# Kernel optimization log

Hardware: AMD Instinct MI355X
Metric: run time of the kernel (lower is better)

Reference implementation:

```python
import jax, jax.numpy as jnp
import numpy as np
from jax import lax

B, L = 4, 1024
D_MODEL = 512
D_INNER = 2 * D_MODEL            # expand=2 -> 1024
HEADDIM = 64
NHEADS = D_INNER // HEADDIM      # 16
D_STATE = 64
D_CONV = 4
NLAYERS = 2
NTOKEN = 60695
PAD_IDX = 60694
NCLS = 164
CONV_DIM = D_INNER + 2 * D_STATE            # 1152 (ngroups=1)
D_IN_PROJ = 2 * D_INNER + 2 * D_STATE + NHEADS  # 2192
MAX_VALUE = 512.0
EPS = 1e-5


def _ln(x, g=None, b=None):
    m = jnp.mean(x, -1, keepdims=True)
    v = jnp.mean((x - m) ** 2, -1, keepdims=True)
    y = (x - m) * lax.rsqrt(v + EPS)
    return y if g is None else y * g + b


def _smart_flip(X, pad_mask):
    # reverse only the valid (non-pad) prefix of each sequence
    lengths = (~pad_mask).sum(1)
    rng = jnp.arange(X.shape[1])[None, :]
    flip = rng < lengths[:, None]
    pos = jnp.where(flip, lengths[:, None] - 1 - rng, rng)
    return jnp.take_along_axis(X, pos[:, :, None], axis=1)


def _mamba2(u, in_w, conv_w, conv_b, A_log, dt_bias, Dskip, norm_w, out_w):
    # Mamba2 block (mamba_ssm defaults: ngroups=1, silu conv act, gated RMSNorm)
    Bb, Ll, _ = u.shape
    zxbcdt = u @ in_w.T                                      # (B,L,D_IN_PROJ)
    z = zxbcdt[..., :D_INNER]
    xBC = zxbcdt[..., D_INNER:D_INNER + CONV_DIM]
    dt = jax.nn.softplus(zxbcdt[..., -NHEADS:] + dt_bias)    # (B,L,H)
    # causal depthwise conv1d + silu
    xBC = jnp.pad(xBC, ((0, 0), (D_CONV - 1, 0), (0, 0))).transpose(0, 2, 1)
    xBC = lax.conv_general_dilated(xBC, conv_w[:, None, :], (1,), 'VALID',
                                   feature_group_count=CONV_DIM)
    xBC = jax.nn.silu(xBC.transpose(0, 2, 1) + conv_b)       # (B,L,CONV_DIM)
    x = xBC[..., :D_INNER].reshape(Bb, Ll, NHEADS, HEADDIM)
    Bm = xBC[..., D_INNER:D_INNER + D_STATE]                 # (B,L,N)
    Cm = xBC[..., D_INNER + D_STATE:]                        # (B,L,N)
    dA = jnp.exp(dt * (-jnp.exp(A_log)))                     # (B,L,H)

    def step(h, t):
        dA_t, dt_t, x_t, B_t, C_t = t
        # h: (B,H,P,N)
        h = h * dA_t[:, :, None, None] \
            + (dt_t[:, :, None] * x_t)[..., None] * B_t[:, None, None, :]
        y = jnp.einsum('bhpn,bn->bhp', h, C_t)
        return h, y

    h0 = jnp.zeros((Bb, NHEADS, HEADDIM, D_STATE), u.dtype)
    xs = (dA.transpose(1, 0, 2), dt.transpose(1, 0, 2),
          x.transpose(1, 0, 2, 3), Bm.transpose(1, 0, 2), Cm.transpose(1, 0, 2))
    _, ys = lax.scan(step, h0, xs)                            # (L,B,H,P)
    y = ys.transpose(1, 0, 2, 3) + Dskip[None, None, :, None] * x
    y = y.reshape(Bb, Ll, D_INNER)
    y = y * jax.nn.silu(z)                                    # gated RMSNorm
    y = y * lax.rsqrt(jnp.mean(y * y, -1, keepdims=True) + EPS) * norm_w
    return y @ out_w.T


def _forward(src, values, pad_mask, embed, ge_ln_g, ge_ln_b,
             ve_w1, ve_b1, ve_w2, ve_b2, ve_ln_g, ve_ln_b,
             in_proj_w, conv_w_f, conv_b_f, A_log_f, dt_bias_f, D_f, norm_w_f,
             conv_w_r, conv_b_r, A_log_r, dt_bias_r, D_r, norm_w_r, out_proj_w,
             expr_w1, expr_b1, expr_w2, expr_b2, expr_w3, expr_b3,
             cls_w1, cls_b1, cls_ln1_g, cls_ln1_b, cls_w2, cls_b2,
             cls_ln2_g, cls_ln2_b, cls_wo, cls_bo):
    src_emb = _ln(embed[src], ge_ln_g, ge_ln_b)
    v = jnp.minimum(values, MAX_VALUE)[..., None]
    v = jax.nn.relu(v @ ve_w1.T + ve_b1)
    v = _ln(v @ ve_w2.T + ve_b2, ve_ln_g, ve_ln_b)
    h = (src_emb + v) * (~pad_mask)[..., None]
    for i in range(NLAYERS):
        hn = _ln(h)  # F.layer_norm without affine
        out = _mamba2(hn, in_proj_w[i], conv_w_f[i], conv_b_f[i], A_log_f[i],
                      dt_bias_f[i], D_f[i], norm_w_f[i], out_proj_w[i])
        rev = _smart_flip(hn, pad_mask)
        out_r = _mamba2(rev, in_proj_w[i], conv_w_r[i], conv_b_r[i], A_log_r[i],
                        dt_bias_r[i], D_r[i], norm_w_r[i], out_proj_w[i])
        out_r = _smart_flip(out_r, pad_mask)
        h = _ln((out + out_r) / 2)
    # ExprDecoder (MLM head)
    e = jax.nn.leaky_relu(h @ expr_w1.T + expr_b1)
    e = jax.nn.leaky_relu(e @ expr_w2.T + expr_b2)
    mlm = (e @ expr_w3.T + expr_b3)[..., 0]
    # cell embedding: cls token
    cell = h[:, 0, :]
    # ClsDecoder
    c = _ln(jax.nn.relu(cell @ cls_w1.T + cls_b1), cls_ln1_g, cls_ln1_b)
    c = _ln(jax.nn.relu(c @ cls_w2.T + cls_b2), cls_ln2_g, cls_ln2_b)
    cls = c @ cls_wo.T + cls_bo
    return mlm, cell, cls


def setup_inputs() -> dict:
    key = jax.random.key(0)
    ks = iter(jax.random.split(key, 64))
    w = lambda *s: jax.random.normal(next(ks), s, jnp.float32) * 0.02
    embed = w(NTOKEN, D_MODEL).at[PAD_IDX].set(0.0)
    dt_u = jax.random.uniform(next(ks), (NLAYERS, NHEADS), minval=1e-3, maxval=0.1)
    dt_u2 = jax.random.uniform(next(ks), (NLAYERS, NHEADS), minval=1e-3, maxval=0.1)
    return dict(
        src=jax.random.randint(next(ks), (B, L), 0, PAD_IDX),
        values=jax.random.uniform(next(ks), (B, L), jnp.float32),
        src_key_padding_mask=jnp.zeros((B, L), bool),
        embed=embed,
        ge_ln_g=jnp.ones((D_MODEL,)), ge_ln_b=jnp.zeros((D_MODEL,)),
        ve_w1=w(D_MODEL, 1), ve_b1=jnp.zeros((D_MODEL,)),
        ve_w2=w(D_MODEL, D_MODEL), ve_b2=jnp.zeros((D_MODEL,)),
        ve_ln_g=jnp.ones((D_MODEL,)), ve_ln_b=jnp.zeros((D_MODEL,)),
        in_proj_w=w(NLAYERS, D_IN_PROJ, D_MODEL),
        conv_w_f=w(NLAYERS, CONV_DIM, D_CONV), conv_b_f=jnp.zeros((NLAYERS, CONV_DIM)),
        A_log_f=jnp.log(jax.random.uniform(next(ks), (NLAYERS, NHEADS), minval=1.0, maxval=16.0)),
        dt_bias_f=dt_u + jnp.log(-jnp.expm1(-dt_u)),
        D_f=jnp.ones((NLAYERS, NHEADS)), norm_w_f=jnp.ones((NLAYERS, D_INNER)),
        conv_w_r=w(NLAYERS, CONV_DIM, D_CONV), conv_b_r=jnp.zeros((NLAYERS, CONV_DIM)),
        A_log_r=jnp.log(jax.random.uniform(next(ks), (NLAYERS, NHEADS), minval=1.0, maxval=16.0)),
        dt_bias_r=dt_u2 + jnp.log(-jnp.expm1(-dt_u2)),
        D_r=jnp.ones((NLAYERS, NHEADS)), norm_w_r=jnp.ones((NLAYERS, D_INNER)),
        out_proj_w=w(NLAYERS, D_MODEL, D_INNER),
        expr_w1=w(D_MODEL, D_MODEL), expr_b1=jnp.zeros((D_MODEL,)),
        expr_w2=w(D_MODEL, D_MODEL), expr_b2=jnp.zeros((D_MODEL,)),
        expr_w3=w(1, D_MODEL), expr_b3=jnp.zeros((1,)),
        cls_w1=w(D_MODEL, D_MODEL), cls_b1=jnp.zeros((D_MODEL,)),
        cls_ln1_g=jnp.ones((D_MODEL,)), cls_ln1_b=jnp.zeros((D_MODEL,)),
        cls_w2=w(D_MODEL, D_MODEL), cls_b2=jnp.zeros((D_MODEL,)),
        cls_ln2_g=jnp.ones((D_MODEL,)), cls_ln2_b=jnp.zeros((D_MODEL,)),
        cls_wo=w(NCLS, D_MODEL), cls_bo=jnp.zeros((NCLS,)),
    )


def reference(src, values, src_key_padding_mask, embed, ge_ln_g, ge_ln_b,
              ve_w1, ve_b1, ve_w2, ve_b2, ve_ln_g, ve_ln_b,
              in_proj_w, conv_w_f, conv_b_f, A_log_f, dt_bias_f, D_f, norm_w_f,
              conv_w_r, conv_b_r, A_log_r, dt_bias_r, D_r, norm_w_r, out_proj_w,
              expr_w1, expr_b1, expr_w2, expr_b2, expr_w3, expr_b3,
              cls_w1, cls_b1, cls_ln1_g, cls_ln1_b, cls_w2, cls_b2,
              cls_ln2_g, cls_ln2_b, cls_wo, cls_bo):
    return _forward(src, values, src_key_padding_mask, embed, ge_ln_g, ge_ln_b,
                    ve_w1, ve_b1, ve_w2, ve_b2, ve_ln_g, ve_ln_b,
                    in_proj_w, conv_w_f, conv_b_f, A_log_f, dt_bias_f, D_f, norm_w_f,
                    conv_w_r, conv_b_r, A_log_r, dt_bias_r, D_r, norm_w_r, out_proj_w,
                    expr_w1, expr_b1, expr_w2, expr_b2, expr_w3, expr_b3,
                    cls_w1, cls_b1, cls_ln1_g, cls_ln1_b, cls_w2, cls_b2,
                    cls_ln2_g, cls_ln2_b, cls_wo, cls_bo)
```

## Files before the change

kernel.cpp:

```cpp
#include <hip/hip_runtime.h>
#include <hip/hip_bf16.h>
#include <math.h>

constexpr int Bb = 4, Ls = 1024, DM = 512, DI = 1024, NH = 16, HD = 64, DS = 64;
constexpr int CDIM = DI + 2 * DS;
constexpr int DIP  = 2 * DI + 2 * DS + NH;
constexpr int NPJ  = 2 * DI + 2 * DS;
constexpr float EPSf = 1e-5f;
constexpr int TOK = Bb * Ls;
constexpr int CH = 64, NCH = Ls / CH;

#define DEVI __device__ __forceinline__

using bfrag = __attribute__((ext_vector_type(8))) short;
using f4v   = __attribute__((ext_vector_type(4))) float;
using u16x8 = __attribute__((ext_vector_type(8))) unsigned short;

#define GLOAD16(gp, lp)                                                              \
  __builtin_amdgcn_global_load_lds((__attribute__((address_space(1))) void*)(gp),   \
                                   (__attribute__((address_space(3))) void*)(lp),   \
                                   16, 0, 0)

DEVI float wsum(float v) {
#pragma unroll
  for (int o = 32; o > 0; o >>= 1) v += __shfl_xor(v, o);
  return v;
}
DEVI float sigmoidf_(float x) { return 1.f / (1.f + __expf(-x)); }
DEVI unsigned short f2bf(float x) {
  union { float f; unsigned u; } c{x};
  unsigned u = c.u;
  u += 0x7fffu + ((u >> 16) & 1u);
  return (unsigned short)(u >> 16);
}
DEVI float bf2f(unsigned short u) {
  union { unsigned u; float f; } c{(unsigned)u << 16};
  return c.f;
}

DEVI void ld8(const float* __restrict__ p, int lane, float (&x)[8]) {
  float4 a = *(const float4*)(p + lane * 4);
  float4 b = *(const float4*)(p + 256 + lane * 4);
  x[0] = a.x; x[1] = a.y; x[2] = a.z; x[3] = a.w;
  x[4] = b.x; x[5] = b.y; x[6] = b.z; x[7] = b.w;
}
DEVI void ld8bf(const unsigned short* __restrict__ p, int lane, float (&x)[8]) {
  ushort4 a = *(const ushort4*)(p + lane * 4);
  ushort4 b = *(const ushort4*)(p + 256 + lane * 4);
  x[0] = bf2f(a.x); x[1] = bf2f(a.y); x[2] = bf2f(a.z); x[3] = bf2f(a.w);
  x[4] = bf2f(b.x); x[5] = bf2f(b.y); x[6] = bf2f(b.z); x[7] = bf2f(b.w);
}
DEVI void st8(float* __restrict__ p, int lane, const float (&x)[8]) {
  *(float4*)(p + lane * 4) = make_float4(x[0], x[1], x[2], x[3]);
  *(float4*)(p + 256 + lane * 4) = make_float4(x[4], x[5], x[6], x[7]);
}
DEVI void st8bf(unsigned short* __restrict__ p, int lane, const float (&x)[8]) {
  *(ushort4*)(p + lane * 4) = make_ushort4(f2bf(x[0]), f2bf(x[1]), f2bf(x[2]), f2bf(x[3]));
  *(ushort4*)(p + 256 + lane * 4) = make_ushort4(f2bf(x[4]), f2bf(x[5]), f2bf(x[6]), f2bf(x[7]));
}
DEVI void norm8(float (&x)[8]) {
  float s = 0;
#pragma unroll
  for (int j = 0; j < 8; ++j) s += x[j];
  float mean = wsum(s) * (1.f / 512.f);
#pragma unroll
  for (int j = 0; j < 8; ++j) x[j] -= mean;
  float q = 0;
#pragma unroll
  for (int j = 0; j < 8; ++j) q += x[j] * x[j];
  float var = wsum(q) * (1.f / 512.f);
  float inv = rsqrtf(var + EPSf);
#pragma unroll
  for (int j = 0; j < 8; ++j) x[j] *= inv;
}

__global__ __launch_bounds__(256) void k_w2bf(const float* __restrict__ in,
                                              unsigned short* __restrict__ out, int n8) {
  int i = blockIdx.x * 256 + threadIdx.x;
  if (i >= n8) return;
  const float4* p = (const float4*)in + (size_t)i * 2;
  float4 a = p[0], b = p[1];
  *((ushort4*)out + (size_t)i * 2) = make_ushort4(f2bf(a.x), f2bf(a.y), f2bf(a.z), f2bf(a.w));
  *((ushort4*)out + (size_t)i * 2 + 1) = make_ushort4(f2bf(b.x), f2bf(b.y), f2bf(b.z), f2bf(b.w));
}

__global__ __launch_bounds__(256) void k_embed(const int* __restrict__ src, const float* __restrict__ values,
    const float* __restrict__ embed, const float* __restrict__ gg, const float* __restrict__ gb,
    const float* __restrict__ vw1, const float* __restrict__ vb1,
    float* __restrict__ hbuf, unsigned short* __restrict__ v1bf) {
  int gw = (blockIdx.x * 256 + threadIdx.x) >> 6;
  int lane = threadIdx.x & 63;
  if (gw >= TOK) return;
  const float* er = embed + (size_t)src[gw] * DM;
  float x[8];
  ld8(er, lane, x);
  norm8(x);
  float g[8], bv[8];
  ld8(gg, lane, g); ld8(gb, lane, bv);
#pragma unroll
  for (int j = 0; j < 8; ++j) x[j] = x[j] * g[j] + bv[j];
  st8(hbuf + (size_t)gw * DM, lane, x);
  float val = fminf(values[gw], 512.f);
  float w1[8], b1[8];
  ld8(vw1, lane, w1); ld8(vb1, lane, b1);
  float v[8];
#pragma unroll
  for (int j = 0; j < 8; ++j) v[j] = fmaxf(val * w1[j] + b1[j], 0.f);
  st8bf(v1bf + (size_t)gw * DM, lane, v);
}

__global__ __launch_bounds__(256) void k_haddv(const float* __restrict__ t2, const float* __restrict__ g,
    const float* __restrict__ bb, const unsigned char* __restrict__ mask, float* __restrict__ hbuf) {
  int gw = (blockIdx.x * 256 + threadIdx.x) >> 6;
  int lane = threadIdx.x & 63;
  if (gw >= TOK) return;
  float x[8];
  ld8(t2 + (size_t)gw * DM, lane, x);
  norm8(x);
  float gv[8], bv[8], h[8];
  ld8(g, lane, gv); ld8(bb, lane, bv);
  ld8(hbuf + (size_t)gw * DM, lane, h);
  float mf = mask[gw] ? 0.f : 1.f;
#pragma unroll
  for (int j = 0; j < 8; ++j) h[j] = (h[j] + x[j] * gv[j] + bv[j]) * mf;
  st8(hbuf + (size_t)gw * DM, lane, h);
}

__global__ __launch_bounds__(256) void k_lndt(const float* __restrict__ h, const float* __restrict__ inw,
    const float* __restrict__ dtbF, const float* __restrict__ AlogF,
    const float* __restrict__ dtbR, const float* __restrict__ AlogR,
    const int* __restrict__ len, unsigned short* __restrict__ hnbf,
    float* __restrict__ dtf, float* __restrict__ laf,
    float* __restrict__ dtr, float* __restrict__ lar) {
  int gw = (blockIdx.x * 256 + threadIdx.x) >> 6;
  int lane = threadIdx.x & 63;
  if (gw >= TOK) return;
  float x[8];
  ld8(h + (size_t)gw * DM, lane, x);
  norm8(x);
  st8bf(hnbf + (size_t)gw * DM, lane, x);
  const float* wdt = inw + (size_t)NPJ * DM;
  float myraw = 0.f;
#pragma unroll
  for (int hh = 0; hh < NH; ++hh) {
    float w[8];
    ld8(wdt + (size_t)hh * DM, lane, w);
    float s = 0;
#pragma unroll
    for (int j = 0; j < 8; ++j) s += x[j] * w[j];
    s = wsum(s);
    if (lane == hh) myraw = s;
  }
  if (lane < NH) {
    int t = gw & (Ls - 1), b = gw >> 10;
    int ln = len[b];
    int pos = (t < ln) ? (ln - 1 - t) : t;
    size_t grev = (size_t)(b * Ls + pos);
    float rf = myraw + dtbF[lane];
    float df = rf > 20.f ? rf : log1pf(__expf(rf));
    dtf[(size_t)gw * NH + lane] = df;
    laf[(size_t)gw * NH + lane] = -__expf(AlogF[lane]) * df;
    float rr = myraw + dtbR[lane];
    float dr = rr > 20.f ? rr : log1pf(__expf(rr));
    dtr[grev * NH + lane] = dr;
    lar[grev * NH + lane] = -__expf(AlogR[lane]) * dr;
  }
}

template <int ACT, int OMODE>
__global__ __launch_bounds__(256) void gemm_bf(const unsigned short* __restrict__ A,
    const unsigned short* __restrict__ W, const float* __restrict__ bias,
    void* __restrict__ Cout, int M, int N, int K) {
  constexpr int BK = 64;
  __shared__ unsigned short As[128 * BK];
  __shared__ unsigned short Bs[128 * BK];
  int tid = threadIdx.x;
  int bm = blockIdx.y * 128, bn = blockIdx.x * 128;
  int wv = tid >> 6, lane = tid & 63;
  int mb = (wv >> 1) * 64, nb = (wv & 1) * 64;
  int rA = lane >> 3;
  int cswz = (lane & 7) ^ rA;
  f4v acc[4][4] = {};

  for (int k0 = 0; k0 < K; k0 += BK) {
#pragma unroll
    for (int q = 0; q < 4; ++q) {
      int ch = wv * 4 + q;
      const unsigned short* ga = A + (size_t)(bm + ch * 8 + rA) * K + k0 + cswz * 8;
      GLOAD16(ga, &As[ch * 512]);
      const unsigned short* gb = W + (size_t)(bn + ch * 8 + rA) * K + k0 + cswz * 8;
      GLOAD16(gb, &Bs[ch * 512]);
    }
    __syncthreads();
#pragma unroll
    for (int ks = 0; ks < BK; ks += 32) {
      int kb = (ks >> 3) + (lane >> 4);
      bfrag af[4], bg[4];
#pragma unroll
      for (int i = 0; i < 4; ++i) {
        int ra_ = mb + i * 16 + (lane & 15);
        af[i] = *(const bfrag*)((const char*)As + ((ra_ * 128 + kb * 16) ^ ((ra_ & 7) << 4)));
        int rb_ = nb + i * 16 + (lane & 15);
        bg[i] = *(const bfrag*)((const char*)Bs + ((rb_ * 128 + kb * 16) ^ ((rb_ & 7) << 4)));
      }
#pragma unroll
      for (int i = 0; i < 4; ++i)
#pragma unroll
        for (int j = 0; j < 4; ++j)
          acc[i][j] = __builtin_amdgcn_mfma_f32_16x16x32_bf16(af[i], bg[j], acc[i][j], 0, 0, 0);
    }
    __syncthreads();
  }

  int cb = bn + nb + (lane & 15);
  int rb = bm + mb + ((lane >> 4) << 2);
#pragma unroll
  for (int j = 0; j < 4; ++j) {
    float bv = bias ? bias[cb + j * 16] : 0.f;
#pragma unroll
    for (int i = 0; i < 4; ++i) {
#pragma unroll
      for (int r = 0; r < 4; ++r) {
        float v = acc[i][j][r] + bv;
        if (ACT == 1) v = fmaxf(v, 0.f);
        if (ACT == 2) v = v > 0.f ? v : 0.01f * v;
        size_t idx = (size_t)(rb + i * 16 + r) * N + cb + j * 16;
        if (OMODE == 0) ((float*)Cout)[idx] = v;
        else ((unsigned short*)Cout)[idx] = f2bf(v);
      }
    }
  }
}

__global__ __launch_bounds__(256) void k_convbc(const unsigned short* __restrict__ zx,
    const float* __restrict__ cwF, const float* __restrict__ cbF,
    const float* __restrict__ cwR, const float* __restrict__ cbR,
    const int* __restrict__ len, unsigned short* __restrict__ bcbuf) {
  int idx = blockIdx.x * 256 + threadIdx.x;
  if (idx >= 2 * TOK * 128) return;
  int col = idx & 127;
  int bt = (idx >> 7) & (TOK - 1);
  int dir = idx >> 19;
  int b = bt >> 10, t = bt & (Ls - 1);
  int ln = len[b];
  const float* cw = dir ? cwR : cwF;
  const float* cb = dir ? cbR : cbF;
  int ccd = DI + col;
  float4 w4 = *(const float4*)(cw + ccd * 4);
  float s = cb[ccd];
  float wk[4] = {w4.x, w4.y, w4.z, w4.w};
#pragma unroll
  for (int k = 0; k < 4; ++k) {
    int rl = t - 3 + k;
    if (rl >= 0) {
      int gr = dir ? (rl < ln ? ln - 1 - rl : rl) : rl;
      s += wk[k] * bf2f(zx[((size_t)(b * Ls + gr)) * NPJ + 2 * DI + col]);
    }
  }
  s = s * sigmoidf_(s);
  bcbuf[idx] = f2bf(s);
}

__global__ __launch_bounds__(256) void k_chunk(const unsigned short* __restrict__ zx,
    const unsigned short* __restrict__ bcbuf,
    const float* __restrict__ cwF, const float* __restrict__ cbF,
    const float* __restrict__ cwR, const float* __restrict__ cbR,
    const float* __restrict__ dtF, const float* __restrict__ laF,
    const float* __restrict__ dtR, const float* __restrict__ laR,
    const float* __restrict__ DkF, const float* __restrict__ DkR,
    const int* __restrict__ len,
    float* __restrict__ yF, float* __restrict__ yR,
    float* __restrict__ gbuf, float* __restrict__ cumbuf) {
  __shared__ unsigned short Cb[4096], Bbs[4096], BbT[4096], xT[4096], Wt[4096];
  __shared__ float ldsL[64], sdt_[64], fs[64];
  int blk2 = blockIdx.x;
  int dir = blk2 >> 10;
  int blk = blk2 & 1023;
  int c = blk & 15, bh = blk >> 4, h = bh & 15, b = bh >> 4;
  int tid = threadIdx.x, wv = tid >> 6, lane = tid & 63;
  int c0 = c * CH;
  int ln = len[b];
  const float* cw = dir ? cwR : cwF;
  const float* cbias = dir ? cbR : cbF;
  const float* dtp = dir ? dtR : dtF;
  const float* ldap = dir ? laR : laF;
  float Dh = (dir ? DkR : DkF)[h];
  float* y = dir ? yR : yF;

  if (tid < 64) {
    size_t off = ((size_t)(b * Ls + c0 + tid)) * NH + h;
    float dtv = dtp[off];
    float v = ldap[off];
#pragma unroll
    for (int o = 1; o < 64; o <<= 1) {
      float n = __shfl_up(v, o);
      if (tid >= o) v += n;
    }
    ldsL[tid] = v;
    sdt_[tid] = dtv;
    cumbuf[(size_t)blk2 * 64 + tid] = __expf(v);
    float L63 = __shfl(v, 63);
    fs[tid] = __expf(L63 - v) * dtv;
  }
  __syncthreads();

  {
    const unsigned short* bc = bcbuf + ((size_t)(dir * TOK + b * Ls + c0)) * 128;
    int r = tid >> 2;
    int colq = (tid & 3) * 32;
#pragma unroll
    for (int g = 0; g < 2; ++g) {
      int col = colq + g * 16;
      u16x8 v0 = *(const u16x8*)(bc + (size_t)r * 128 + col);
      u16x8 v1 = *(const u16x8*)(bc + (size_t)r * 128 + col + 8);
      if (col < 64) {
        *(u16x8*)((char*)Bbs + ((r * 128 + col * 2) ^ ((r & 7) << 4))) = v0;
        *(u16x8*)((char*)Bbs + ((r * 128 + col * 2 + 16) ^ ((r & 7) << 4))) = v1;
      } else {
        int n = col - 64;
        *(u16x8*)((char*)Cb + ((r * 128 + n * 2) ^ ((r & 7) << 4))) = v0;
        *(u16x8*)((char*)Cb + ((r * 128 + n * 2 + 16) ^ ((r & 7) << 4))) = v1;
      }
    }
  }
  {
    int n = tid & 63;
    int tg = (tid >> 6) * 16;
    const unsigned short* bc = bcbuf + ((size_t)(dir * TOK + b * Ls + c0 + tg)) * 128 + n;
    float vals[16];
#pragma unroll
    for (int t = 0; t < 16; ++t) vals[t] = bf2f(bc[(size_t)t * 128]) * fs[tg + t];
#pragma unroll
    for (int hv = 0; hv < 2; ++hv) {
      u16x8 pk;
#pragma unroll
      for (int k = 0; k < 8; ++k) pk[k] = f2bf(vals[hv * 8 + k]);
      *(u16x8*)((char*)BbT + ((n * 128 + (tg + hv * 8) * 2) ^ ((n & 7) << 4))) = pk;
    }
  }
  {
    int cch = tid & 63;
    int tg = (tid >> 6) * 16;
    int gcol = DI + h * 64 + cch;
    int ccd = h * 64 + cch;
    float4 w4 = *(const float4*)(cw + ccd * 4);
    float bias = cbias[ccd];
    float vv[19];
#pragma unroll
    for (int k = 0; k < 19; ++k) {
      int rl = c0 + tg - 3 + k;
      float val = 0.f;
      if (rl >= 0) {
        int gr = dir ? (rl < ln ? ln - 1 - rl : rl) : rl;
        val = bf2f(zx[((size_t)(b * Ls + gr)) * NPJ + gcol]);
      }
      vv[k] = val;
    }
    int p = cch;
#pragma unroll
    for (int hv = 0; hv < 2; ++hv) {
      u16x8 pk;
#pragma unroll
      for (int k = 0; k < 8; ++k) {
        int t = hv * 8 + k;
        float s = bias + w4.x * vv[t] + w4.y * vv[t + 1] + w4.z * vv[t + 2] + w4.w * vv[t + 3];
        pk[k] = f2bf(s * sigmoidf_(s));
      }
      *(u16x8*)((char*)xT + ((p * 128 + (tg + hv * 8) * 2) ^ ((p & 7) << 4))) = pk;
    }
  }
  __syncthreads();

  f4v accS[4] = {};
#pragma unroll
  for (int ks = 0; ks < 64; ks += 32) {
    int kb = (ks >> 3) + (lane >> 4);
    int ra = wv * 16 + (lane & 15);
    bfrag af = *(const bfrag*)((const char*)Cb + ((ra * 128 + kb * 16) ^ ((ra & 7) << 4)));
#pragma unroll
    for (int j = 0; j < 4; ++j) {
      int rb = j * 16 + (lane & 15);
      bfrag bg = *(const bfrag*)((const char*)Bbs + ((rb * 128 + kb * 16) ^ ((rb & 7) << 4)));
      accS[j] = __builtin_amdgcn_mfma_f32_16x16x32_bf16(af, bg, accS[j], 0, 0, 0);
    }
  }
  {
    int trow = wv * 16 + ((lane >> 4) << 2);
#pragma unroll
    for (int j = 0; j < 4; ++j) {
      int s = j * 16 + (lane & 15);
      float ds = sdt_[s], Lsv = ldsL[s];
#pragma unroll
      for (int r = 0; r < 4; ++r) {
        int tt = trow + r;
        float wval = (s <= tt) ? accS[j][r] * ds * __expf(ldsL[tt] - Lsv) : 0.f;
        *(unsigned short*)((char*)Wt + ((tt * 128 + s * 2) ^ ((tt & 7) << 4))) = f2bf(wval);
      }
    }
  }
  __syncthreads();

  f4v accY[4] = {}, accG[4] = {};
#pragma unroll
  for (int ks = 0; ks < 64; ks += 32) {
    int kb = (ks >> 3) + (lane >> 4);
    int ra = wv * 16 + (lane & 15);
    bfrag afW = *(const bfrag*)((const char*)Wt + ((ra * 128 + kb * 16) ^ ((ra & 7) << 4)));
    bfrag afB = *(const bfrag*)((const char*)BbT + ((ra * 128 + kb * 16) ^ ((ra & 7) << 4)));
#pragma unroll
    for (int j = 0; j < 4; ++j) {
      int rb = j * 16 + (lane & 15);
      bfrag bg = *(const bfrag*)((const char*)xT + ((rb * 128 + kb * 16) ^ ((rb & 7) << 4)));
      accY[j] = __builtin_amdgcn_mfma_f32_16x16x32_bf16(afW, bg, accY[j], 0, 0, 0);
      accG[j] = __builtin_amdgcn_mfma_f32_16x16x32_bf16(afB, bg, accG[j], 0, 0, 0);
    }
  }
  int trow = wv * 16 + ((lane >> 4) << 2);
#pragma unroll
  for (int j = 0; j < 4; ++j) {
    int p = j * 16 + (lane & 15);
#pragma unroll
    for (int r = 0; r < 4; ++r) {
      int t = trow + r;
      float xval = bf2f(*(const unsigned short*)((const char*)xT + ((p * 128 + t * 2) ^ ((p & 7) << 4))));
      y[((size_t)(b * Ls + c0 + t)) * DI + h * 64 + p] = accY[j][r] + Dh * xval;
      gbuf[((size_t)blk2 * 64 + t) * 64 + p] = accG[j][r];
    }
  }
}

__global__ __launch_bounds__(256) void k_chain(float* __restrict__ gbuf, const float* __restrict__ cumbuf) {
  int bh = blockIdx.x;
  int tid = threadIdx.x;
  size_t base = (size_t)bh * NCH * 4096;
  float4 hv[4] = {};
  float4 g[4], gn[4];
#pragma unroll
  for (int k = 0; k < 4; ++k) g[k] = *(const float4*)(gbuf + base + (size_t)k * 1024 + tid * 4);
  float Pc = cumbuf[(size_t)bh * NCH * 64 + 63];
  for (int c = 0; c < NCH; ++c) {
    float Pn = 0.f;
    if (c + 1 < NCH) {
      Pn = cumbuf[((size_t)bh * NCH + c + 1) * 64 + 63];
#pragma unroll
      for (int k = 0; k < 4; ++k)
        gn[k] = *(const float4*)(gbuf + base + (size_t)(c + 1) * 4096 + (size_t)k * 1024 + tid * 4);
    }
#pragma unroll
    for (int k = 0; k < 4; ++k) {
      *(float4*)(gbuf + base + (size_t)c * 4096 + (size_t)k * 1024 + tid * 4) = hv[k];
      hv[k].x = fmaf(Pc, hv[k].x, g[k].x);
      hv[k].y = fmaf(Pc, hv[k].y, g[k].y);
      hv[k].z = fmaf(Pc, hv[k].z, g[k].z);
      hv[k].w = fmaf(Pc, hv[k].w, g[k].w);
      g[k] = gn[k];
    }
    Pc = Pn;
  }
}

__global__ __launch_bounds__(256) void k_corr(const unsigned short* __restrict__ bcbuf,
    const float* __restrict__ hin, const float* __restrict__ cumbuf,
    float* __restrict__ yF, float* __restrict__ yR) {
  int blk2 = blockIdx.x;
  int c = blk2 & 15;
  if (c == 0) return;
  __shared__ unsigned short Ct[4096], HT[4096];
  __shared__ float cdl[64];
  int dir = blk2 >> 10;
  int bh = (blk2 & 1023) >> 4, h = bh & 15, b = bh >> 4;
  int tid = threadIdx.x, wv = tid >> 6, lane = tid & 63;
  int c0 = c * CH;
  float* y = dir ? yR : yF;
  {
    int r = tid >> 2;
    int colq = (tid & 3) * 16;
    const unsigned short* bc = bcbuf + ((size_t)(dir * TOK + b * Ls + c0 + r)) * 128 + 64 + colq;
    u16x8 v0 = *(const u16x8*)bc;
    u16x8 v1 = *(const u16x8*)(bc + 8);
    *(u16x8*)((char*)Ct + ((r * 128 + colq * 2) ^ ((r & 7) << 4))) = v0;
    *(u16x8*)((char*)Ct + ((r * 128 + colq * 2 + 16) ^ ((r & 7) << 4))) = v1;
  }
  {
    int n = tid >> 2, p0 = (tid & 3) * 16;
    const float* hr = hin + (size_t)blk2 * 4096 + (size_t)n * 64 + p0;
#pragma unroll
    for (int q = 0; q < 4; ++q) {
      float4 v = *(const float4*)(hr + q * 4);
      float va[4] = {v.x, v.y, v.z, v.w};
#pragma unroll
      for (int k = 0; k < 4; ++k) {
        int p = p0 + q * 4 + k;
        *(unsigned short*)((char*)HT + ((p * 128 + n * 2) ^ ((p & 7) << 4))) = f2bf(va[k]);
      }
    }
  }
  if (tid < 64) cdl[tid] = cumbuf[(size_t)blk2 * 64 + tid];
  __syncthreads();

  f4v acc[4] = {};
#pragma unroll
  for (int ks = 0; ks < 64; ks += 32) {
    int kb = (ks >> 3) + (lane >> 4);
    int ra = wv * 16 + (lane & 15);
    bfrag af = *(const bfrag*)((const char*)Ct + ((ra * 128 + kb * 16) ^ ((ra & 7) << 4)));
#pragma unroll
    for (int j = 0; j < 4; ++j) {
      int rb = j * 16 + (lane & 15);
      bfrag bg = *(const bfrag*)((const char*)HT + ((rb * 128 + kb * 16) ^ ((rb & 7) << 4)));
      acc[j] = __builtin_amdgcn_mfma_f32_16x16x32_bf16(af, bg, acc[j], 0, 0, 0);
    }
  }
  int trow = wv * 16 + ((lane >> 4) << 2);
#pragma unroll
  for (int j = 0; j < 4; ++j) {
    int p = j * 16 + (lane & 15);
#pragma unroll
    for (int r = 0; r < 4; ++r) {
      int t = trow + r;
      float* yp = &y[((size_t)(b * Ls + c0 + t)) * DI + h * 64 + p];
      *yp += cdl[t] * acc[j][r];
    }
  }
}

__global__ __launch_bounds__(256) void k_gab(const float* __restrict__ yF, const float* __restrict__ yR,
    const unsigned short* __restrict__ zxb, const float* __restrict__ nwF, const float* __restrict__ nwR,
    const int* __restrict__ len, unsigned short* __restrict__ ybf) {
  int w = (blockIdx.x * 256 + threadIdx.x) >> 6;
  int lane = threadIdx.x & 63;
  if (w >= TOK) return;
  int t = w & (Ls - 1), b = w >> 10;
  int ln = len[b];
  int r = b * Ls + ((t < ln) ? (ln - 1 - t) : t);
  const float* yf = yF + (size_t)w * DI;
  const float* yr = yR + (size_t)r * DI;
  const unsigned short* zr = zxb + (size_t)w * NPJ;
  float gf[16], gr[16];
  float ssf = 0.f, ssr = 0.f;
#pragma unroll
  for (int q = 0; q < 4; ++q) {
    float4 yv = *(const float4*)(yf + lane * 4 + q * 256);
    float4 rv = *(const float4*)(yr + lane * 4 + q * 256);
    ushort4 zu = *(const ushort4*)(zr + lane * 4 + q * 256);
    float z0 = bf2f(zu.x), z1 = bf2f(zu.y), z2 = bf2f(zu.z), z3 = bf2f(zu.w);
    float s0 = z0 * sigmoidf_(z0), s1 = z1 * sigmoidf_(z1), s2 = z2 * sigmoidf_(z2), s3 = z3 * sigmoidf_(z3);
    gf[4 * q + 0] = yv.x * s0; gf[4 * q + 1] = yv.y * s1; gf[4 * q + 2] = yv.z * s2; gf[4 * q + 3] = yv.w * s3;
    gr[4 * q + 0] = rv.x * s0; gr[4 * q + 1] = rv.y * s1; gr[4 * q + 2] = rv.z * s2; gr[4 * q + 3] = rv.w * s3;
#pragma unroll
    for (int j = 0; j < 4; ++j) {
      ssf += gf[4 * q + j] * gf[4 * q + j];
      ssr += gr[4 * q + j] * gr[4 * q + j];
    }
  }
  ssf = wsum(ssf);
  ssr = wsum(ssr);
  float scf = 0.5f * rsqrtf(ssf * (1.f / (float)DI) + EPSf);
  float scr = 0.5f * rsqrtf(ssr * (1.f / (float)DI) + EPSf);
#pragma unroll
  for (int q = 0; q < 4; ++q) {
    float4 nf = *(const float4*)(nwF + lane * 4 + q * 256);
    float4 nr = *(const float4*)(nwR + lane * 4 + q * 256);
    float o0 = gf[4 * q + 0] * scf * nf.x + gr[4 * q + 0] * scr * nr.x;
    float o1 = gf[4 * q + 1] * scf * nf.y + gr[4 * q + 1] * scr * nr.y;
    float o2 = gf[4 * q + 2] * scf * nf.z + gr[4 * q + 2] * scr * nr.z;
    float o3 = gf[4 * q + 3] * scf * nf.w + gr[4 * q + 3] * scr * nr.w;
    *(ushort4*)(ybf + (size_t)w * DI + lane * 4 + q * 256) =
        make_ushort4(f2bf(o0), f2bf(o1), f2bf(o2), f2bf(o3));
  }
}

__global__ __launch_bounds__(256) void k_hln(const float* __restrict__ src, float* __restrict__ dst,
                                             unsigned short* __restrict__ dstbf) {
  int gw = (blockIdx.x * 256 + threadIdx.x) >> 6;
  int lane = threadIdx.x & 63;
  if (gw >= TOK) return;
  float x[8];
  ld8(src + (size_t)gw * DM, lane, x);
  norm8(x);
  st8(dst + (size_t)gw * DM, lane, x);
  st8bf(dstbf + (size_t)gw * DM, lane, x);
}

__global__ __launch_bounds__(256) void k_lengths(const unsigned char* __restrict__ mask, int* __restrict__ len) {
  int b = blockIdx.x;
  int tid = threadIdx.x;
  int cnt = 0;
  for (int t = tid; t < Ls; t += 256) cnt += mask[b * Ls + t] ? 0 : 1;
#pragma unroll
  for (int o = 32; o > 0; o >>= 1) cnt += __shfl_xor(cnt, o);
  __shared__ int red[4];
  if ((tid & 63) == 0) red[tid >> 6] = cnt;
  __syncthreads();
  if (tid == 0) len[b] = red[0] + red[1] + red[2] + red[3];
}

__global__ __launch_bounds__(256) void k_mlm(const unsigned short* __restrict__ e2,
                                             const float* __restrict__ w3,
                                             const float* __restrict__ b3, float* __restrict__ out) {
  int gw = (blockIdx.x * 256 + threadIdx.x) >> 6;
  int lane = threadIdx.x & 63;
  if (gw >= TOK) return;
  float x[8], w[8];
  ld8bf(e2 + (size_t)gw * DM, lane, x);
  ld8(w3, lane, w);
  float s = 0;
#pragma unroll
  for (int j = 0; j < 8; ++j) s += x[j] * w[j];
  s = wsum(s);
  if (lane == 0) out[gw] = s + b3[0];
}

__global__ __launch_bounds__(256) void k_cell(const float* __restrict__ h, float* __restrict__ out) {
  int i = blockIdx.x * 256 + threadIdx.x;
  if (i >= Bb * DM) return;
  int b = i >> 9, c = i & 511;
  out[i] = h[(size_t)b * Ls * DM + c];
}

__global__ __launch_bounds__(256) void k_clsmv(const float* __restrict__ xin, size_t xstride,
    const float* __restrict__ g, const float* __restrict__ bb, int doLN,
    const float* __restrict__ W, const float* __restrict__ bias, int doRelu,
    float* __restrict__ out, int nout) {
  int b = blockIdx.y;
  int j = blockIdx.x * 4 + (threadIdx.x >> 6);
  int lane = threadIdx.x & 63;
  if (j >= nout) return;
  float x[8];
  ld8(xin + (size_t)b * xstride, lane, x);
  if (doLN) {
    norm8(x);
    float gv[8], bv[8];
    ld8(g, lane, gv); ld8(bb, lane, bv);
#pragma unroll
    for (int k = 0; k < 8; ++k) x[k] = x[k] * gv[k] + bv[k];
  }
  float w[8];
  ld8(W + (size_t)j * DM, lane, w);
  float s = 0;
#pragma unroll
  for (int k = 0; k < 8; ++k) s += x[k] * w[k];
  s = wsum(s);
  if (lane == 0) {
    float v = s + bias[j];
    if (doRelu) v = fmaxf(v, 0.f);
    out[(size_t)b * nout + j] = v;
  }
}

constexpr size_t F_H   = 0;
constexpr size_t F_DTF = F_H + (size_t)TOK * DM;
constexpr size_t F_LAF = F_DTF + (size_t)TOK * NH;
constexpr size_t F_DTR = F_LAF + (size_t)TOK * NH;
constexpr size_t F_LAR = F_DTR + (size_t)TOK * NH;
constexpr size_t F_YF  = F_LAR + (size_t)TOK * NH;
constexpr size_t F_YR  = F_YF + (size_t)TOK * DI;
constexpr size_t F_ON  = F_YR + (size_t)TOK * DI;
constexpr size_t F_G   = F_ON + (size_t)TOK * DM;
constexpr size_t F_CUM = F_G + (size_t)2 * Bb * NH * NCH * HD * DS;
constexpr size_t F_CC1 = F_CUM + (size_t)2 * Bb * NH * NCH * 64;
constexpr size_t F_CC2 = F_CC1 + Bb * DM;
constexpr size_t F_LEN = F_CC2 + Bb * DM;
constexpr size_t F_END = F_LEN + 16;
constexpr size_t U0     = F_END * 2;
constexpr size_t UW_IN  = U0;
constexpr size_t UW_OUT = UW_IN + (size_t)2 * DIP * DM;
constexpr size_t UW_VE  = UW_OUT + (size_t)2 * DM * DI;
constexpr size_t UW_E1  = UW_VE + (size_t)DM * DM;
constexpr size_t UW_E2  = UW_E1 + (size_t)DM * DM;
constexpr size_t U_BFA  = UW_E2 + (size_t)DM * DM;
constexpr size_t U_HNBF = U_BFA + (size_t)TOK * DM;
constexpr size_t U_YBF  = U_HNBF + (size_t)TOK * DM;
constexpr size_t U_ZX   = U_YBF + (size_t)TOK * DI;
constexpr size_t U_BC   = U_ZX + (size_t)TOK * NPJ;

extern "C" void kernel_launch(void* const* d_in, const int* in_sizes, int n_in,
                              void* d_out, int out_size, void* d_ws, size_t ws_size,
                              hipStream_t stream) {
  const int* src = (const int*)d_in[0];
  const float* values = (const float*)d_in[1];
  const unsigned char* mask = (const unsigned char*)d_in[2];
  const float* embed = (const float*)d_in[3];
  const float* ge_g = (const float*)d_in[4];
  const float* ge_b = (const float*)d_in[5];
  const float* ve_w1 = (const float*)d_in[6];
  const float* ve_b1 = (const float*)d_in[7];
  const float* ve_w2 = (const float*)d_in[8];
  const float* ve_b2 = (const float*)d_in[9];
  const float* ve_g = (const float*)d_in[10];
  const float* ve_bb = (const float*)d_in[11];
  const float* in_w = (const float*)d_in[12];
  const float* conv_w_f = (const float*)d_in[13];
  const float* conv_b_f = (const float*)d_in[14];
  const float* A_f = (const float*)d_in[15];
  const float* dtb_f = (const float*)d_in[16];
  const float* D_f = (const float*)d_in[17];
  const float* nw_f = (const float*)d_in[18];
  const float* conv_w_r = (const float*)d_in[19];
  const float* conv_b_r = (const float*)d_in[20];
  const float* A_r = (const float*)d_in[21];
  const float* dtb_r = (const float*)d_in[22];
  const float* D_r = (const float*)d_in[23];
  const float* nw_r = (const float*)d_in[24];
  const float* out_w = (const float*)d_in[25];
  const float* expr_w1 = (const float*)d_in[26];
  const float* expr_b1 = (const float*)d_in[27];
  const float* expr_w2 = (const float*)d_in[28];
  const float* expr_b2 = (const float*)d_in[29];
  const float* expr_w3 = (const float*)d_in[30];
  const float* expr_b3 = (const float*)d_in[31];
  const float* cls_w1 = (const float*)d_in[32];
  const float* cls_b1 = (const float*)d_in[33];
  const float* cls_g1 = (const float*)d_in[34];
  const float* cls_bb1 = (const float*)d_in[35];
  const float* cls_w2 = (const float*)d_in[36];
  const float* cls_b2 = (const float*)d_in[37];
  const float* cls_g2 = (const float*)d_in[38];
  const float* cls_bb2 = (const float*)d_in[39];
  const float* cls_wo = (const float*)d_in[40];
  const float* cls_bo = (const float*)d_in[41];

  float* ws = (float*)d_ws;
  unsigned short* wsu = (unsigned short*)d_ws;
  float* h = ws + F_H;
  float* dtf = ws + F_DTF;
  float* laf = ws + F_LAF;
  float* dtr = ws + F_DTR;
  float* lar = ws + F_LAR;
  float* yF = ws + F_YF;
  float* yR = ws + F_YR;
  float* onew = ws + F_ON;
  float* gbuf = ws + F_G;
  float* cumb = ws + F_CUM;
  float* cc1 = ws + F_CC1;
  float* cc2 = ws + F_CC2;
  int* len = (int*)(ws + F_LEN);
  unsigned short* w_in = wsu + UW_IN;
  unsigned short* w_out = wsu + UW_OUT;
  unsigned short* w_ve = wsu + UW_VE;
  unsigned short* w_e1 = wsu + UW_E1;
  unsigned short* w_e2 = wsu + UW_E2;
  unsigned short* bfa = wsu + U_BFA;
  unsigned short* hnbf = wsu + U_HNBF;
  unsigned short* ybf = wsu + U_YBF;
  unsigned short* zxb = wsu + U_ZX;
  unsigned short* bcbuf = wsu + U_BC;
  float* t2 = onew;
  unsigned short* e2b = zxb;
  float* out = (float*)d_out;

  {
    int n;
    n = 2 * DIP * DM / 8;  k_w2bf<<<(n + 255) / 256, 256, 0, stream>>>(in_w, w_in, n);
    n = 2 * DM * DI / 8;   k_w2bf<<<(n + 255) / 256, 256, 0, stream>>>(out_w, w_out, n);
    n = DM * DM / 8;       k_w2bf<<<(n + 255) / 256, 256, 0, stream>>>(ve_w2, w_ve, n);
    n = DM * DM / 8;       k_w2bf<<<(n + 255) / 256, 256, 0, stream>>>(expr_w1, w_e1, n);
    n = DM * DM / 8;       k_w2bf<<<(n + 255) / 256, 256, 0, stream>>>(expr_w2, w_e2, n);
  }

  k_embed<<<TOK / 4, 256, 0, stream>>>(src, values, embed, ge_g, ge_b, ve_w1, ve_b1, h, bfa);
  gemm_bf<0, 0><<<dim3(DM / 128, TOK / 128), 256, 0, stream>>>(bfa, w_ve, ve_b2, t2, TOK, DM, DM);
  k_haddv<<<TOK / 4, 256, 0, stream>>>(t2, ve_g, ve_bb, mask, h);
  k_lengths<<<Bb, 256, 0, stream>>>(mask, len);

  for (int i = 0; i < 2; ++i) {
    const float* inw = in_w + (size_t)i * DIP * DM;
    unsigned short* inwb = w_in + (size_t)i * DIP * DM;
    unsigned short* outwb = w_out + (size_t)i * DM * DI;
    const float* cwF = conv_w_f + (size_t)i * CDIM * 4;
    const float* cbF = conv_b_f + (size_t)i * CDIM;
    const float* cwR = conv_w_r + (size_t)i * CDIM * 4;
    const float* cbR = conv_b_r + (size_t)i * CDIM;
    k_lndt<<<TOK / 4, 256, 0, stream>>>(h, inw, dtb_f + i * NH, A_f + i * NH,
                                        dtb_r + i * NH, A_r + i * NH, len, hnbf,
                                        dtf, laf, dtr, lar);
    gemm_bf<0, 1><<<dim3(NPJ / 128, TOK / 128), 256, 0, stream>>>(hnbf, inwb, nullptr, zxb, TOK, NPJ, DM);
    k_convbc<<<(2 * TOK * 128) / 256, 256, 0, stream>>>(zxb, cwF, cbF, cwR, cbR, len, bcbuf);
    k_chunk<<<2 * Bb * NH * NCH, 256, 0, stream>>>(zxb, bcbuf, cwF, cbF, cwR, cbR,
        dtf, laf, dtr, lar, D_f + i * NH, D_r + i * NH, len, yF, yR, gbuf, cumb);
    k_chain<<<2 * Bb * NH, 256, 0, stream>>>(gbuf, cumb);
    k_corr<<<2 * Bb * NH * NCH, 256, 0, stream>>>(bcbuf, gbuf, cumb, yF, yR);
    k_gab<<<TOK / 4, 256, 0, stream>>>(yF, yR, zxb, nw_f + (size_t)i * DI, nw_r + (size_t)i * DI,
                                       len, ybf);
    gemm_bf<0, 0><<<dim3(DM / 128, TOK / 128), 256, 0, stream>>>(ybf, outwb, nullptr, onew, TOK, DM, DI);
    k_hln<<<TOK / 4, 256, 0, stream>>>(onew, h, hnbf);
  }

  gemm_bf<2, 1><<<dim3(DM / 128, TOK / 128), 256, 0, stream>>>(hnbf, w_e1, expr_b1, bfa, TOK, DM, DM);
  gemm_bf<2, 1><<<dim3(DM / 128, TOK / 128), 256, 0, stream>>>(bfa, w_e2, expr_b2, e2b, TOK, DM, DM);
  k_mlm<<<TOK / 4, 256, 0, stream>>>(e2b, expr_w3, expr_b3, out);
  k_cell<<<(Bb * DM + 255) / 256, 256, 0, stream>>>(h, out + TOK);
  k_clsmv<<<dim3(128, Bb), 256, 0, stream>>>(h, (size_t)Ls * DM, nullptr, nullptr, 0,
                                             cls_w1, cls_b1, 1, cc1, DM);
  k_clsmv<<<dim3(128, Bb), 256, 0, stream>>>(cc1, DM, cls_g1, cls_bb1, 1,
                                             cls_w2, cls_b2, 1, cc2, DM);
  k_clsmv<<<dim3(41, Bb), 256, 0, stream>>>(cc2, DM, cls_g2, cls_bb2, 1,
                                            cls_wo, cls_bo, 0, out + TOK + Bb * DM, 164);
}
```

Measured before the change: 347.9 us.

## Store SSM outputs and chunk states in bf16 and drop redundant fp32 hidden writes

Changes the per-direction SSM outputs yF/yR and the inter-chunk state buffer gbuf from fp32 to bf16 across k_chunk, k_chain, k_corr and k_gab, halving their memory traffic. The fp32 write of the normalized hidden state after each layer is removed. The next layer's LN reads onew directly, and the final norm for the cell output is recomputed only for the rows that need it. The bcbuf workspace is aliased onto ybf. Keeping intermediate y values and the chained states in bf16 adds rounding error, including a read-modify-write in bf16 in k_corr.

```diff
diff --git a/kernel.cpp b/kernel.cpp
--- a/kernel.cpp
+++ b/kernel.cpp
@@ -126,7 +126,7 @@
   st8(hbuf + (size_t)gw * DM, lane, h);
 }
 
-__global__ __launch_bounds__(256) void k_lndt(const float* __restrict__ h, const float* __restrict__ inw,
+__global__ __launch_bounds__(256) void k_lndt(const float* __restrict__ pre, const float* __restrict__ inw,
     const float* __restrict__ dtbF, const float* __restrict__ AlogF,
     const float* __restrict__ dtbR, const float* __restrict__ AlogR,
     const int* __restrict__ len, unsigned short* __restrict__ hnbf,
@@ -136,7 +136,7 @@
   int lane = threadIdx.x & 63;
   if (gw >= TOK) return;
   float x[8];
-  ld8(h + (size_t)gw * DM, lane, x);
+  ld8(pre + (size_t)gw * DM, lane, x);
   norm8(x);
   st8bf(hnbf + (size_t)gw * DM, lane, x);
   const float* wdt = inw + (size_t)NPJ * DM;
@@ -269,8 +269,8 @@
     const float* __restrict__ dtR, const float* __restrict__ laR,
     const float* __restrict__ DkF, const float* __restrict__ DkR,
     const int* __restrict__ len,
-    float* __restrict__ yF, float* __restrict__ yR,
-    float* __restrict__ gbuf, float* __restrict__ cumbuf) {
+    unsigned short* __restrict__ yF, unsigned short* __restrict__ yR,
+    unsigned short* __restrict__ gbuf, float* __restrict__ cumbuf) {
   __shared__ unsigned short Cb[4096], Bbs[4096], BbT[4096], xT[4096], Wt[4096];
   __shared__ float ldsL[64], sdt_[64], fs[64];
   int blk2 = blockIdx.x;
@@ -285,7 +285,7 @@
   const float* dtp = dir ? dtR : dtF;
   const float* ldap = dir ? laR : laF;
   float Dh = (dir ? DkR : DkF)[h];
-  float* y = dir ? yR : yF;
+  unsigned short* y = dir ? yR : yF;
 
   if (tid < 64) {
     size_t off = ((size_t)(b * Ls + c0 + tid)) * NH + h;
@@ -423,45 +423,47 @@
     for (int r = 0; r < 4; ++r) {
       int t = trow + r;
       float xval = bf2f(*(const unsigned short*)((const char*)xT + ((p * 128 + t * 2) ^ ((p & 7) << 4))));
-      y[((size_t)(b * Ls + c0 + t)) * DI + h * 64 + p] = accY[j][r] + Dh * xval;
-      gbuf[((size_t)blk2 * 64 + t) * 64 + p] = accG[j][r];
-    }
-  }
-}
-
-__global__ __launch_bounds__(256) void k_chain(float* __restrict__ gbuf, const float* __restrict__ cumbuf) {
+      y[((size_t)(b * Ls + c0 + t)) * DI + h * 64 + p] = f2bf(accY[j][r] + Dh * xval);
+      gbuf[((size_t)blk2 * 64 + t) * 64 + p] = f2bf(accG[j][r]);
+    }
+  }
+}
+
+__global__ __launch_bounds__(256) void k_chain(unsigned short* __restrict__ gbuf,
+                                               const float* __restrict__ cumbuf) {
   int bh = blockIdx.x;
   int tid = threadIdx.x;
-  size_t base = (size_t)bh * NCH * 4096;
-  float4 hv[4] = {};
-  float4 g[4], gn[4];
-#pragma unroll
-  for (int k = 0; k < 4; ++k) g[k] = *(const float4*)(gbuf + base + (size_t)k * 1024 + tid * 4);
+  size_t base = (size_t)bh * NCH * 4096 + (size_t)tid * 16;
+  float hv[16] = {};
+  u16x8 ga = *(const u16x8*)(gbuf + base);
+  u16x8 gb_ = *(const u16x8*)(gbuf + base + 8);
   float Pc = cumbuf[(size_t)bh * NCH * 64 + 63];
   for (int c = 0; c < NCH; ++c) {
+    u16x8 na = {}, nb = {};
     float Pn = 0.f;
     if (c + 1 < NCH) {
       Pn = cumbuf[((size_t)bh * NCH + c + 1) * 64 + 63];
-#pragma unroll
-      for (int k = 0; k < 4; ++k)
-        gn[k] = *(const float4*)(gbuf + base + (size_t)(c + 1) * 4096 + (size_t)k * 1024 + tid * 4);
-    }
-#pragma unroll
-    for (int k = 0; k < 4; ++k) {
-      *(float4*)(gbuf + base + (size_t)c * 4096 + (size_t)k * 1024 + tid * 4) = hv[k];
-      hv[k].x = fmaf(Pc, hv[k].x, g[k].x);
-      hv[k].y = fmaf(Pc, hv[k].y, g[k].y);
-      hv[k].z = fmaf(Pc, hv[k].z, g[k].z);
-      hv[k].w = fmaf(Pc, hv[k].w, g[k].w);
-      g[k] = gn[k];
-    }
+      na = *(const u16x8*)(gbuf + base + (size_t)(c + 1) * 4096);
+      nb = *(const u16x8*)(gbuf + base + (size_t)(c + 1) * 4096 + 8);
+    }
+    u16x8 oa, ob;
+#pragma unroll
+    for (int k = 0; k < 8; ++k) { oa[k] = f2bf(hv[k]); ob[k] = f2bf(hv[8 + k]); }
+    *(u16x8*)(gbuf + base + (size_t)c * 4096) = oa;
+    *(u16x8*)(gbuf + base + (size_t)c * 4096 + 8) = ob;
+#pragma unroll
+    for (int k = 0; k < 8; ++k) {
+      hv[k] = fmaf(Pc, hv[k], bf2f(ga[k]));
+      hv[8 + k] = fmaf(Pc, hv[8 + k], bf2f(gb_[k]));
+    }
+    ga = na; gb_ = nb;
     Pc = Pn;
   }
 }
 
 __global__ __launch_bounds__(256) void k_corr(const unsigned short* __restrict__ bcbuf,
-    const float* __restrict__ hin, const float* __restrict__ cumbuf,
-    float* __restrict__ yF, float* __restrict__ yR) {
+    const unsigned short* __restrict__ gbuf, const float* __restrict__ cumbuf,
+    unsigned short* __restrict__ yF, unsigned short* __restrict__ yR) {
   int blk2 = blockIdx.x;
   int c = blk2 & 15;
   if (c == 0) return;
@@ -471,7 +473,7 @@
   int bh = (blk2 & 1023) >> 4, h = bh & 15, b = bh >> 4;
   int tid = threadIdx.x, wv = tid >> 6, lane = tid & 63;
   int c0 = c * CH;
-  float* y = dir ? yR : yF;
+  unsigned short* y = dir ? yR : yF;
   {
     int r = tid >> 2;
     int colq = (tid & 3) * 16;
@@ -483,16 +485,15 @@
   }
   {
     int n = tid >> 2, p0 = (tid & 3) * 16;
-    const float* hr = hin + (size_t)blk2 * 4096 + (size_t)n * 64 + p0;
-#pragma unroll
-    for (int q = 0; q < 4; ++q) {
-      float4 v = *(const float4*)(hr + q * 4);
-      float va[4] = {v.x, v.y, v.z, v.w};
-#pragma unroll
-      for (int k = 0; k < 4; ++k) {
-        int p = p0 + q * 4 + k;
-        *(unsigned short*)((char*)HT + ((p * 128 + n * 2) ^ ((p & 7) << 4))) = f2bf(va[k]);
-      }
+    const unsigned short* hr = gbuf + (size_t)blk2 * 4096 + (size_t)n * 64 + p0;
+    u16x8 v0 = *(const u16x8*)hr;
+    u16x8 v1 = *(const u16x8*)(hr + 8);
+#pragma unroll
+    for (int k = 0; k < 8; ++k) {
+      int p = p0 + k;
+      *(unsigned short*)((char*)HT + ((p * 128 + n * 2) ^ ((p & 7) << 4))) = v0[k];
+      int p2 = p0 + 8 + k;
+      *(unsigned short*)((char*)HT + ((p2 * 128 + n * 2) ^ ((p2 & 7) << 4))) = v1[k];
     }
   }
   if (tid < 64) cdl[tid] = cumbuf[(size_t)blk2 * 64 + tid];
@@ -518,14 +519,15 @@
 #pragma unroll
     for (int r = 0; r < 4; ++r) {
       int t = trow + r;
-      float* yp = &y[((size_t)(b * Ls + c0 + t)) * DI + h * 64 + p];
-      *yp += cdl[t] * acc[j][r];
-    }
-  }
-}
-
-__global__ __launch_bounds__(256) void k_gab(const float* __restrict__ yF, const float* __restrict__ yR,
-    const unsigned short* __restrict__ zxb, const float* __restrict__ nwF, const float* __restrict__ nwR,
+      unsigned short* yp = &y[((size_t)(b * Ls + c0 + t)) * DI + h * 64 + p];
+      *yp = f2bf(bf2f(*yp) + cdl[t] * acc[j][r]);
+    }
+  }
+}
+
+__global__ __launch_bounds__(256) void k_gab(const unsigned short* __restrict__ yF,
+    const unsigned short* __restrict__ yR, const unsigned short* __restrict__ zxb,
+    const float* __restrict__ nwF, const float* __restrict__ nwR,
     const int* __restrict__ len, unsigned short* __restrict__ ybf) {
   int w = (blockIdx.x * 256 + threadIdx.x) >> 6;
   int lane = threadIdx.x & 63;
@@ -533,20 +535,22 @@
   int t = w & (Ls - 1), b = w >> 10;
   int ln = len[b];
   int r = b * Ls + ((t < ln) ? (ln - 1 - t) : t);
-  const float* yf = yF + (size_t)w * DI;
-  const float* yr = yR + (size_t)r * DI;
+  const unsigned short* yf = yF + (size_t)w * DI;
+  const unsigned short* yr = yR + (size_t)r * DI;
   const unsigned short* zr = zxb + (size_t)w * NPJ;
   float gf[16], gr[16];
   float ssf = 0.f, ssr = 0.f;
 #pragma unroll
   for (int q = 0; q < 4; ++q) {
-    float4 yv = *(const float4*)(yf + lane * 4 + q * 256);
-    float4 rv = *(const float4*)(yr + lane * 4 + q * 256);
+    ushort4 yv = *(const ushort4*)(yf + lane * 4 + q * 256);
+    ushort4 rv = *(const ushort4*)(yr + lane * 4 + q * 256);
     ushort4 zu = *(const ushort4*)(zr + lane * 4 + q * 256);
     float z0 = bf2f(zu.x), z1 = bf2f(zu.y), z2 = bf2f(zu.z), z3 = bf2f(zu.w);
     float s0 = z0 * sigmoidf_(z0), s1 = z1 * sigmoidf_(z1), s2 = z2 * sigmoidf_(z2), s3 = z3 * sigmoidf_(z3);
-    gf[4 * q + 0] = yv.x * s0; gf[4 * q + 1] = yv.y * s1; gf[4 * q + 2] = yv.z * s2; gf[4 * q + 3] = yv.w * s3;
-    gr[4 * q + 0] = rv.x * s0; gr[4 * q + 1] = rv.y * s1; gr[4 * q + 2] = rv.z * s2; gr[4 * q + 3] = rv.w * s3;
+    gf[4 * q + 0] = bf2f(yv.x) * s0; gf[4 * q + 1] = bf2f(yv.y) * s1;
+    gf[4 * q + 2] = bf2f(yv.z) * s2; gf[4 * q + 3] = bf2f(yv.w) * s3;
+    gr[4 * q + 0] = bf2f(rv.x) * s0; gr[4 * q + 1] = bf2f(rv.y) * s1;
+    gr[4 * q + 2] = bf2f(rv.z) * s2; gr[4 * q + 3] = bf2f(rv.w) * s3;
 #pragma unroll
     for (int j = 0; j < 4; ++j) {
       ssf += gf[4 * q + j] * gf[4 * q + j];
@@ -570,7 +574,7 @@
   }
 }
 
-__global__ __launch_bounds__(256) void k_hln(const float* __restrict__ src, float* __restrict__ dst,
+__global__ __launch_bounds__(256) void k_hl2(const float* __restrict__ src,
                                              unsigned short* __restrict__ dstbf) {
   int gw = (blockIdx.x * 256 + threadIdx.x) >> 6;
   int lane = threadIdx.x & 63;
@@ -578,7 +582,6 @@
   float x[8];
   ld8(src + (size_t)gw * DM, lane, x);
   norm8(x);
-  st8(dst + (size_t)gw * DM, lane, x);
   st8bf(dstbf + (size_t)gw * DM, lane, x);
 }
 
@@ -611,11 +614,15 @@
   if (lane == 0) out[gw] = s + b3[0];
 }
 
-__global__ __launch_bounds__(256) void k_cell(const float* __restrict__ h, float* __restrict__ out) {
-  int i = blockIdx.x * 256 + threadIdx.x;
-  if (i >= Bb * DM) return;
-  int b = i >> 9, c = i & 511;
-  out[i] = h[(size_t)b * Ls * DM + c];
+__global__ __launch_bounds__(256) void k_cell(const float* __restrict__ onew, float* __restrict__ out,
+                                              float* __restrict__ cc0) {
+  int b = threadIdx.x >> 6;
+  int lane = threadIdx.x & 63;
+  float x[8];
+  ld8(onew + (size_t)b * Ls * DM, lane, x);
+  norm8(x);
+  st8(out + (size_t)b * DM, lane, x);
+  st8(cc0 + (size_t)b * DM, lane, x);
 }
 
 __global__ __launch_bounds__(256) void k_clsmv(const float* __restrict__ xin, size_t xstride,
@@ -653,12 +660,10 @@
 constexpr size_t F_LAF = F_DTF + (size_t)TOK * NH;
 constexpr size_t F_DTR = F_LAF + (size_t)TOK * NH;
 constexpr size_t F_LAR = F_DTR + (size_t)TOK * NH;
-constexpr size_t F_YF  = F_LAR + (size_t)TOK * NH;
-constexpr size_t F_YR  = F_YF + (size_t)TOK * DI;
-constexpr size_t F_ON  = F_YR + (size_t)TOK * DI;
-constexpr size_t F_G   = F_ON + (size_t)TOK * DM;
-constexpr size_t F_CUM = F_G + (size_t)2 * Bb * NH * NCH * HD * DS;
-constexpr size_t F_CC1 = F_CUM + (size_t)2 * Bb * NH * NCH * 64;
+constexpr size_t F_ON  = F_LAR + (size_t)TOK * NH;
+constexpr size_t F_CUM = F_ON + (size_t)TOK * DM;
+constexpr size_t F_CC0 = F_CUM + (size_t)2 * Bb * NH * NCH * 64;
+constexpr size_t F_CC1 = F_CC0 + Bb * DM;
 constexpr size_t F_CC2 = F_CC1 + Bb * DM;
 constexpr size_t F_LEN = F_CC2 + Bb * DM;
 constexpr size_t F_END = F_LEN + 16;
@@ -672,7 +677,9 @@
 constexpr size_t U_HNBF = U_BFA + (size_t)TOK * DM;
 constexpr size_t U_YBF  = U_HNBF + (size_t)TOK * DM;
 constexpr size_t U_ZX   = U_YBF + (size_t)TOK * DI;
-constexpr size_t U_BC   = U_ZX + (size_t)TOK * NPJ;
+constexpr size_t U_YF   = U_ZX + (size_t)TOK * NPJ;
+constexpr size_t U_YR   = U_YF + (size_t)TOK * DI;
+constexpr size_t U_G    = U_YR + (size_t)TOK * DI;
 
 extern "C" void kernel_launch(void* const* d_in, const int* in_sizes, int n_in,
                               void* d_out, int out_size, void* d_ws, size_t ws_size,
@@ -727,11 +734,9 @@
   float* laf = ws + F_LAF;
   float* dtr = ws + F_DTR;
   float* lar = ws + F_LAR;
-  float* yF = ws + F_YF;
-  float* yR = ws + F_YR;
   float* onew = ws + F_ON;
-  float* gbuf = ws + F_G;
   float* cumb = ws + F_CUM;
+  float* cc0 = ws + F_CC0;
   float* cc1 = ws + F_CC1;
   float* cc2 = ws + F_CC2;
   int* len = (int*)(ws + F_LEN);
@@ -744,7 +749,10 @@
   unsigned short* hnbf = wsu + U_HNBF;
   unsigned short* ybf = wsu + U_YBF;
   unsigned short* zxb = wsu + U_ZX;
-  unsigned short* bcbuf = wsu + U_BC;
+  unsigned short* yFb = wsu + U_YF;
+  unsigned short* yRb = wsu + U_YR;
+  unsigned short* gbuf = wsu + U_G;
+  unsigned short* bcbuf = ybf;
   float* t2 = onew;
   unsigned short* e2b = zxb;
   float* out = (float*)d_out;
@@ -771,26 +779,27 @@
     const float* cbF = conv_b_f + (size_t)i * CDIM;
     const float* cwR = conv_w_r + (size_t)i * CDIM * 4;
     const float* cbR = conv_b_r + (size_t)i * CDIM;
-    k_lndt<<<TOK / 4, 256, 0, stream>>>(h, inw, dtb_f + i * NH, A_f + i * NH,
+    const float* pre = (i == 0) ? h : onew;
+    k_lndt<<<TOK / 4, 256, 0, stream>>>(pre, inw, dtb_f + i * NH, A_f + i * NH,
                                         dtb_r + i * NH, A_r + i * NH, len, hnbf,
                                         dtf, laf, dtr, lar);
     gemm_bf<0, 1><<<dim3(NPJ / 128, TOK / 128), 256, 0, stream>>>(hnbf, inwb, nullptr, zxb, TOK, NPJ, DM);
     k_convbc<<<(2 * TOK * 128) / 256, 256, 0, stream>>>(zxb, cwF, cbF, cwR, cbR, len, bcbuf);
     k_chunk<<<2 * Bb * NH * NCH, 256, 0, stream>>>(zxb, bcbuf, cwF, cbF, cwR, cbR,
-        dtf, laf, dtr, lar, D_f + i * NH, D_r + i * NH, len, yF, yR, gbuf, cumb);
+        dtf, laf, dtr, lar, D_f + i * NH, D_r + i * NH, len, yFb, yRb, gbuf, cumb);
     k_chain<<<2 * Bb * NH, 256, 0, stream>>>(gbuf, cumb);
-    k_corr<<<2 * Bb * NH * NCH, 256, 0, stream>>>(bcbuf, gbuf, cumb, yF, yR);
-    k_gab<<<TOK / 4, 256, 0, stream>>>(yF, yR, zxb, nw_f + (size_t)i * DI, nw_r + (size_t)i * DI,
+    k_corr<<<2 * Bb * NH * NCH, 256, 0, stream>>>(bcbuf, gbuf, cumb, yFb, yRb);
+    k_gab<<<TOK / 4, 256, 0, stream>>>(yFb, yRb, zxb, nw_f + (size_t)i * DI, nw_r + (size_t)i * DI,
                                        len, ybf);
     gemm_bf<0, 0><<<dim3(DM / 128, TOK / 128), 256, 0, stream>>>(ybf, outwb, nullptr, onew, TOK, DM, DI);
-    k_hln<<<TOK / 4, 256, 0, stream>>>(onew, h, hnbf);
-  }
-
+  }
+
+  k_hl2<<<TOK / 4, 256, 0, stream>>>(onew, hnbf);
   gemm_bf<2, 1><<<dim3(DM / 128, TOK / 128), 256, 0, stream>>>(hnbf, w_e1, expr_b1, bfa, TOK, DM, DM);
   gemm_bf<2, 1><<<dim3(DM / 128, TOK / 128), 256, 0, stream>>>(bfa, w_e2, expr_b2, e2b, TOK, DM, DM);
   k_mlm<<<TOK / 4, 256, 0, stream>>>(e2b, expr_w3, expr_b3, out);
-  k_cell<<<(Bb * DM + 255) / 256, 256, 0, stream>>>(h, out + TOK);
-  k_clsmv<<<dim3(128, Bb), 256, 0, stream>>>(h, (size_t)Ls * DM, nullptr, nullptr, 0,
+  k_cell<<<1, 256, 0, stream>>>(onew, out + TOK, cc0);
+  k_clsmv<<<dim3(128, Bb), 256, 0, stream>>>(cc0, DM, nullptr, nullptr, 0,
                                              cls_w1, cls_b1, 1, cc1, DM);
   k_clsmv<<<dim3(128, Bb), 256, 0, stream>>>(cc1, DM, cls_g1, cls_bb1, 1,
                                              cls_w2, cls_b2, 1, cc2, DM);
```

New measurement: 322.2 us. 1.08x faster.
